# Performance work log

Measured on AMD Instinct MI355X. Metric: run time of the kernel, lower is better.

## Reference

```python
import jax, jax.numpy as jnp
import numpy as np

N_EMBD = 1024
N_HEAD = 16

def setup_inputs() -> dict:
    key = jax.random.key(0)
    k0, k1, k2, k3, k4 = jax.random.split(key, 5)
    scale = 1.0 / np.sqrt(N_EMBD)
    x = jax.random.normal(k0, (4, 2048, N_EMBD), dtype=jnp.float32)
    W_qkv = jax.random.normal(k1, (N_EMBD, 3 * N_EMBD), dtype=jnp.float32) * scale
    b_qkv = jax.random.normal(k2, (3 * N_EMBD,), dtype=jnp.float32) * 0.01
    W_proj = jax.random.normal(k3, (N_EMBD, N_EMBD), dtype=jnp.float32) * scale
    b_proj = jax.random.normal(k4, (N_EMBD,), dtype=jnp.float32) * 0.01
    return {"x": x, "W_qkv": W_qkv, "b_qkv": b_qkv, "W_proj": W_proj, "b_proj": b_proj}

def reference(x, W_qkv, b_qkv, W_proj, b_proj):
    B, S, E = x.shape
    H = N_HEAD
    D = E // H  # head dim
    kqv = x @ W_qkv + b_qkv  # [B,S,3E]
    k, q, v = jnp.split(kqv, 3, axis=-1)  # torch split order: k, q, v
    def to_heads(t):
        return t.reshape(B, S, H, D).transpose(0, 2, 1, 3)  # [B,H,S,D]
    k, q, v = to_heads(k), to_heads(q), to_heads(v)
    attn = jnp.einsum('bhqd,bhkd->bhqk', q, k) * (1.0 / np.sqrt(D))
    causal = jnp.tril(jnp.ones((S, S), dtype=bool))
    attn = jnp.where(causal, attn, -jnp.inf)
    attn = jax.nn.softmax(attn, axis=-1)
    # dropout is identity in eval mode (reference baseline)
    y = jnp.einsum('bhqk,bhkd->bhqd', attn, v)
    y = y.transpose(0, 2, 1, 3).reshape(B, S, E)
    return y @ W_proj + b_proj
```

## Files before the change

kernel.cpp:

```cpp
#include <hip/hip_runtime.h>
#include <hip/hip_bf16.h>

typedef __attribute__((ext_vector_type(8))) short  short8;
typedef __attribute__((ext_vector_type(4))) float  f32x4;
typedef __attribute__((ext_vector_type(4))) unsigned short u16x4;
typedef __attribute__((ext_vector_type(2))) unsigned int  uint32x2;

#define WAITVM(n) asm volatile("s_waitcnt vmcnt(" #n ")" ::: "memory")

__device__ __forceinline__ unsigned short f2bf(float f) {
    union { float f; unsigned int u; } c; c.f = f;
    unsigned int u = c.u + 0x7FFFu + ((c.u >> 16) & 1u);
    return (unsigned short)(u >> 16);
}

__device__ __forceinline__ unsigned int cvtpk_bf16(float lo, float hi) {
    unsigned int d;
    asm("v_cvt_pk_bf16_f32 %0, %1, %2" : "=v"(d) : "v"(lo), "v"(hi));
    return d;
}

__device__ __forceinline__ float exp2fast(float x) {
    float r;
    asm("v_exp_f32 %0, %1" : "=v"(r) : "v"(x));
    return r;
}

__device__ __forceinline__ void gll16(const void* g, void* lds) {
    __builtin_amdgcn_global_load_lds(
        (const __attribute__((address_space(1))) unsigned int*)g,
        (__attribute__((address_space(3))) unsigned int*)lds, 16, 0, 0);
}

__global__ void prep_kernel(const float* __restrict__ x, const float* __restrict__ Wq,
                            const float* __restrict__ Wp, unsigned short* __restrict__ xb,
                            unsigned short* __restrict__ WqT, unsigned short* __restrict__ WpT,
                            int nx) {
    const int blk = blockIdx.x;
    if (blk < 4096) {
        __shared__ float tile[32][33];
        const int cx = blk & 127;
        const int k0 = (blk >> 7) * 32;
        const float* W; unsigned short* Wt; int Nd, n0;
        if (cx < 96) { W = Wq; Wt = WqT; Nd = 3072; n0 = cx * 32; }
        else         { W = Wp; Wt = WpT; Nd = 1024; n0 = (cx - 96) * 32; }
        const int tx = threadIdx.x & 31, ty = threadIdx.x >> 5;
#pragma unroll
        for (int i = 0; i < 4; i++)
            tile[ty + i * 8][tx] = W[(size_t)(k0 + ty + i * 8) * Nd + n0 + tx];
        __syncthreads();
#pragma unroll
        for (int i = 0; i < 4; i++)
            Wt[(size_t)(n0 + ty + i * 8) * 1024 + k0 + tx] = f2bf(tile[tx][ty + i * 8]);
    } else {
        int i = ((blk - 4096) * 256 + threadIdx.x) * 4;
        if (i + 3 >= nx) return;
        float4 v = *(const float4*)(x + i);
        u16x4 o;
        o[0] = f2bf(v.x); o[1] = f2bf(v.y); o[2] = f2bf(v.z); o[3] = f2bf(v.w);
        *(u16x4*)(xb + i) = o;
    }
}

template <int BN, int MODE, int NT>
__global__ __launch_bounds__(512, 4) void gemmk64(
    const unsigned short* __restrict__ A,
    const unsigned short* __restrict__ Bt,
    const float* __restrict__ bias,
    float* __restrict__ Cf,
    unsigned short* __restrict__ kbuf,
    unsigned short* __restrict__ qbuf,
    unsigned short* __restrict__ vT,
    int M, int N, int K)
{
    constexpr int NF = BN / 64;
    constexpr int ABASE = 128 * 64;
    constexpr int SLOT = (128 + BN) * 64;
    __shared__ __align__(16) unsigned short lds[2][SLOT];

    const int tid = threadIdx.x;
    const int w = tid >> 6, lane = tid & 63;
    const int llo = lane & 15, lhi = lane >> 4;
    const int wm = w >> 2, wn = w & 3;

    const int nwg = gridDim.x * gridDim.y;
    const int bid = blockIdx.y * gridDim.x + blockIdx.x;
    const int wgid = (bid & 7) * (nwg >> 3) + (bid >> 3);
    const int mb = wgid / gridDim.x, nb = wgid - (wgid / gridDim.x) * gridDim.x;
    const int m0 = mb * 128, n0 = nb * BN;

    f32x4 acc[4][NF];
#pragma unroll
    for (int m = 0; m < 4; m++)
#pragma unroll
        for (int n = 0; n < NF; n++)
#pragma unroll
            for (int r = 0; r < 4; r++) acc[m][n][r] = 0.0f;

    const int gr8 = lane >> 3;
    const int swc = ((lane & 7) ^ gr8) * 8;
    const unsigned short* Asrc = A  + (size_t)(m0 + w * 16 + gr8) * K + swc;
    const unsigned short* Bsrc = Bt + (size_t)(n0 + w * 8 * NF + gr8) * K + swc;

    auto STAGE = [&](int sl_, int kt_) {
        unsigned short* sl = &lds[sl_][0];
        const size_t ko = (size_t)kt_ * 64;
        gll16(Asrc + ko,                 sl + (w * 16) * 64);
        gll16(Asrc + ko + 8 * (size_t)K, sl + (w * 16 + 8) * 64);
#pragma unroll
        for (int u = 0; u < NF; u++)
            gll16(Bsrc + ko + (size_t)(8 * u) * K, sl + ABASE + (w * 8 * NF + 8 * u) * 64);
    };

    STAGE(0, 0);

    const int sk = llo & 7;
    const int arow = (wm * 64 + llo) * 64;
    const int brow = ABASE + (wn * 16 * NF + llo) * 64;

    for (int kt = 0; kt < NT; ++kt) {
        WAITVM(0);
        __builtin_amdgcn_s_barrier();
        __builtin_amdgcn_sched_barrier(0);

        if (kt + 1 < NT) STAGE((kt + 1) & 1, kt + 1);

        const unsigned short* sa = &lds[kt & 1][0];

#pragma unroll
        for (int ks = 0; ks < 2; ks++) {
            const int pc = ((ks * 4 + lhi) ^ sk) * 8;
            short8 af[4], bv[NF];
#pragma unroll
            for (int m = 0; m < 4; m++) af[m] = *(const short8*)&sa[arow + m * 1024 + pc];
#pragma unroll
            for (int n = 0; n < NF; n++) bv[n] = *(const short8*)&sa[brow + n * 1024 + pc];

            __builtin_amdgcn_s_setprio(1);
#pragma unroll
            for (int m = 0; m < 4; m++)
#pragma unroll
                for (int n = 0; n < NF; n++)
                    acc[m][n] = __builtin_amdgcn_mfma_f32_16x16x32_bf16(af[m], bv[n], acc[m][n], 0, 0, 0);
            __builtin_amdgcn_s_setprio(0);
        }
    }

    if constexpr (MODE == 0) {
#pragma unroll
        for (int n = 0; n < NF; n++) {
            int col = n0 + wn * 16 * NF + n * 16 + llo;
            float bb = bias[col];
#pragma unroll
            for (int m = 0; m < 4; m++) {
                int row = m0 + wm * 64 + m * 16 + lhi * 4;
#pragma unroll
                for (int r = 0; r < 4; r++)
                    Cf[(size_t)(row + r) * N + col] = acc[m][n][r] + bb;
            }
        }
    } else {
#pragma unroll
        for (int n = 0; n < NF; n++) {
            int col = n0 + wn * 16 * NF + n * 16 + llo;
            int third = col >> 10;
            int cl  = col & 1023;
            float bb = bias[col];
            if (third == 2) {
#pragma unroll
                for (int m = 0; m < 4; m++) {
                    int row0 = m0 + wm * 64 + m * 16 + lhi * 4;
                    u16x4 pk;
#pragma unroll
                    for (int r = 0; r < 4; r++) pk[r] = f2bf(acc[m][n][r] + bb);
                    *(u16x4*)&vT[(size_t)cl * M + row0] = pk;
                }
            } else {
                unsigned short* dst = (third == 0) ? kbuf : qbuf;
                const float sc = (third == 1) ? 0.18033688f : 1.0f;
#pragma unroll
                for (int m = 0; m < 4; m++) {
                    int row0 = m0 + wm * 64 + m * 16 + lhi * 4;
#pragma unroll
                    for (int r = 0; r < 4; r++)
                        dst[(size_t)(row0 + r) * 1024 + cl] = f2bf((acc[m][n][r] + bb) * sc);
                }
            }
        }
    }
}

__global__ __launch_bounds__(256, 3) void attn_kernel(
    const unsigned short* __restrict__ K_,
    const unsigned short* __restrict__ Q_,
    const unsigned short* __restrict__ VT_,
    unsigned short* __restrict__ O,
    int S, int H, int M)
{
    const int E = 64 * H;
    const int tid = threadIdx.x;
    const int w = tid >> 6, lane = tid & 63;
    const int llo = lane & 15, lhi = lane >> 4;
    const int id = blockIdx.x;
    const int bh = id & 63;
    const int xi = id >> 6;
    const int b = bh >> 4, h = bh & 15;
    const int q0 = (15 - xi) * 128;

    __shared__ __align__(16) unsigned short kvlds[2][2][64 * 64];
    __shared__ __align__(16) unsigned short Ps[4][32 * 64];

    const int qw = q0 + w * 32;

    short8 qf[2][2];
#pragma unroll
    for (int m = 0; m < 2; m++)
#pragma unroll
        for (int kst = 0; kst < 2; kst++)
            qf[m][kst] = *(const short8*)(Q_ + (size_t)(b * S + qw + m * 16 + llo) * E
                                          + h * 64 + kst * 32 + lhi * 8);

    const short one_bf = (short)0x3F80;
    short8 ones = {one_bf, one_bf, one_bf, one_bf, one_bf, one_bf, one_bf, one_bf};

    f32x4 o[2][4];
    f32x4 lac[2];
#pragma unroll
    for (int m = 0; m < 2; m++) {
#pragma unroll
        for (int r = 0; r < 4; r++) lac[m][r] = 0.0f;
#pragma unroll
        for (int df = 0; df < 4; df++)
#pragma unroll
            for (int r = 0; r < 4; r++) o[m][df][r] = 0.0f;
    }

    const int gr = lane >> 3;
    const int gc = ((lane & 7) ^ gr) * 8;
    const unsigned short* ksp = K_  + (size_t)(b * S + w * 16 + gr) * E + h * 64 + gc;
    const unsigned short* vsp = VT_ + (size_t)(h * 64 + w * 16 + gr) * M + b * S + gc;
    unsigned short* kd = &kvlds[0][0][w * 16 * 64];
    unsigned short* vd = &kvlds[0][1][w * 16 * 64];

#define STAGE_KV(buf_, kv0_) {                                   \
        const size_t kro = (size_t)(kv0_) * E;                   \
        gll16(ksp + kro,           kd + (buf_) * 2 * 4096);      \
        gll16(ksp + kro + 8 * (size_t)E, kd + (buf_) * 2 * 4096 + 8 * 64); \
        gll16(vsp + (kv0_),        vd + (buf_) * 2 * 4096);      \
        gll16(vsp + (kv0_) + 8 * M, vd + (buf_) * 2 * 4096 + 8 * 64); \
    }

    STAGE_KV(0, 0);

    const int nt = q0 / 64 + 2;
    unsigned short* psw = &Ps[w][0];

    for (int t = 0; t < nt; ++t) {
        const int kv0 = t * 64;
        WAITVM(0);
        __builtin_amdgcn_s_barrier();
        __builtin_amdgcn_sched_barrier(0);

        if (t + 1 < nt) STAGE_KV((t + 1) & 1, kv0 + 64);

        const unsigned short* kb = &kvlds[t & 1][0][0];
        const unsigned short* vbuf = &kvlds[t & 1][1][0];

        if (kv0 <= qw + 31) {
            f32x4 st[2][4];
#pragma unroll
            for (int m = 0; m < 2; m++)
#pragma unroll
                for (int nf = 0; nf < 4; nf++)
#pragma unroll
                    for (int r = 0; r < 4; r++) st[m][nf][r] = 0.0f;

#pragma unroll
            for (int kst = 0; kst < 2; kst++) {
                const int pc = ((kst * 4 + lhi) ^ (llo & 7)) * 8;
                short8 kf[4];
#pragma unroll
                for (int nf = 0; nf < 4; nf++)
                    kf[nf] = *(const short8*)&kb[(nf * 16 + llo) * 64 + pc];
#pragma unroll
                for (int m = 0; m < 2; m++)
#pragma unroll
                    for (int nf = 0; nf < 4; nf++)
                        st[m][nf] = __builtin_amdgcn_mfma_f32_16x16x32_bf16(kf[nf], qf[m][kst], st[m][nf], 0, 0, 0);
            }

            const bool need_mask = (kv0 + 63 > qw);
#pragma unroll
            for (int m = 0; m < 2; m++) {
                const int qa = qw + m * 16 + llo;
                if (need_mask) {
#pragma unroll
                    for (int nf = 0; nf < 4; nf++)
#pragma unroll
                        for (int r = 0; r < 4; r++) {
                            int ka = kv0 + nf * 16 + lhi * 4 + r;
                            if (ka > qa) st[m][nf][r] = -1e30f;
                        }
                }
#pragma unroll
                for (int nf = 0; nf < 4; nf++) {
                    float p0 = exp2fast(st[m][nf][0]);
                    float p1 = exp2fast(st[m][nf][1]);
                    float p2 = exp2fast(st[m][nf][2]);
                    float p3 = exp2fast(st[m][nf][3]);
                    uint32x2 pk;
                    pk[0] = cvtpk_bf16(p0, p1);
                    pk[1] = cvtpk_bf16(p2, p3);
                    const int p16 = (nf * 2 + (lhi >> 1)) ^ (llo & 7);
                    *(uint32x2*)&psw[(m * 16 + llo) * 64 + p16 * 8 + (lhi & 1) * 4] = pk;
                }
            }

#pragma unroll
            for (int kst = 0; kst < 2; kst++) {
                const int pc = ((kst * 4 + lhi) ^ (llo & 7)) * 8;
                short8 pa[2], vb[4];
#pragma unroll
                for (int m = 0; m < 2; m++)
                    pa[m] = *(const short8*)&psw[(m * 16 + llo) * 64 + pc];
#pragma unroll
                for (int df = 0; df < 4; df++)
                    vb[df] = *(const short8*)&vbuf[(df * 16 + llo) * 64 + pc];
#pragma unroll
                for (int m = 0; m < 2; m++) {
#pragma unroll
                    for (int df = 0; df < 4; df++)
                        o[m][df] = __builtin_amdgcn_mfma_f32_16x16x32_bf16(pa[m], vb[df], o[m][df], 0, 0, 0);
                    lac[m] = __builtin_amdgcn_mfma_f32_16x16x32_bf16(pa[m], ones, lac[m], 0, 0, 0);
                }
            }
        }
    }
#undef STAGE_KV

#pragma unroll
    for (int m = 0; m < 2; m++)
#pragma unroll
        for (int r = 0; r < 4; r++) {
            float iv = 1.0f / lac[m][r];
            int q = qw + m * 16 + lhi * 4 + r;
#pragma unroll
            for (int df = 0; df < 4; df++)
                O[(size_t)(b * S + q) * E + h * 64 + df * 16 + llo] = f2bf(o[m][df][r] * iv);
        }
}

extern "C" void kernel_launch(void* const* d_in, const int* in_sizes, int n_in,
                              void* d_out, int out_size, void* d_ws, size_t ws_size,
                              hipStream_t stream) {
    const float* x      = (const float*)d_in[0];
    const float* W_qkv  = (const float*)d_in[1];
    const float* b_qkv  = (const float*)d_in[2];
    const float* W_proj = (const float*)d_in[3];
    const float* b_proj = (const float*)d_in[4];
    float* out = (float*)d_out;

    const int B = 4, S = 2048, E = 1024, H = 16;
    const int M = B * S;

    unsigned short* ws     = (unsigned short*)d_ws;
    unsigned short* xb     = ws;
    unsigned short* wqkvT  = xb + (size_t)M * E;
    unsigned short* wprojT = wqkvT + (size_t)3 * E * E;
    unsigned short* kbuf   = wprojT + (size_t)E * E;
    unsigned short* qbuf   = kbuf + (size_t)M * E;
    unsigned short* vTb    = qbuf + (size_t)M * E;
    unsigned short* obuf   = vTb + (size_t)M * E;

    const int nx = M * E;
    prep_kernel<<<dim3(4096 + nx / 1024), 256, 0, stream>>>(x, W_qkv, W_proj, xb, wqkvT, wprojT, nx);

    gemmk64<192, 1, 16><<<dim3(3 * E / 192, M / 128), 512, 0, stream>>>(
        xb, wqkvT, b_qkv, nullptr, kbuf, qbuf, vTb, M, 3 * E, E);
    attn_kernel<<<dim3(16 * B * H), 256, 0, stream>>>(kbuf, qbuf, vTb, obuf, S, H, M);
    gemmk64<128, 0, 16><<<dim3(E / 128, M / 128), 512, 0, stream>>>(
        obuf, wprojT, b_proj, out, nullptr, nullptr, nullptr, M, E, E);
}
```

Before: 138.7 us.

## Use 256x256-tile ping-pong GEMM kernel for QKV projection

Adds a new gemm256 kernel with 256x256 output tiles, double-buffered LDS and a fine-grained schedule that interleaves global-to-LDS loads with MFMA groups separated by barriers and raised wave priority. It also remaps workgroup IDs so that neighbouring blocks share operand tiles. It replaces the 128x192 tile kernel for the QKV GEMM to raise arithmetic intensity and overlap memory traffic with compute. The trade-off is more registers and LDS per block, so fewer blocks fit per CU, and a grid of only 384 blocks.

```diff
diff --git a/kernel.cpp b/kernel.cpp
--- a/kernel.cpp
+++ b/kernel.cpp
@@ -61,6 +61,173 @@
         *(u16x4*)(xb + i) = o;
     }
 }
+
+#define SA(b, ko, r) gll16(Asrc + (size_t)((r) * 64) * K + (ko), &lds[b][0][(r) * 4096 + w * 512])
+#define SB(b, ko, r) gll16(Bsrc + (size_t)((r) * 64) * K + (ko), &lds[b][1][(r) * 4096 + w * 512])
+#define BAR __builtin_amdgcn_s_barrier()
+#define LGKM0 { asm volatile("s_waitcnt lgkmcnt(0)" ::: "memory"); __builtin_amdgcn_sched_barrier(0); }
+#define LOADA(ab, MFG) { \
+    _Pragma("unroll") \
+    for (int m_ = 0; m_ < 4; m_++) { \
+        af[m_][0] = *(const short8*)&(ab)[(MFG) * 8192 + arow + m_ * 1024 + pc0]; \
+        af[m_][1] = *(const short8*)&(ab)[(MFG) * 8192 + arow + m_ * 1024 + pc1]; \
+    } }
+#define LOADB(dst, bb, NFG) { \
+    _Pragma("unroll") \
+    for (int n_ = 0; n_ < 2; n_++) { \
+        dst[n_][0] = *(const short8*)&(bb)[((NFG) * 2 + n_) * 4096 + brow + pc0]; \
+        dst[n_][1] = *(const short8*)&(bb)[((NFG) * 2 + n_) * 4096 + brow + pc1]; \
+    } }
+#define MMA(MFG, bv, NFG) { \
+    __builtin_amdgcn_s_setprio(1); \
+    _Pragma("unroll") \
+    for (int m_ = 0; m_ < 4; m_++) \
+        _Pragma("unroll") \
+        for (int n_ = 0; n_ < 2; n_++) { \
+            acc[(MFG) * 4 + m_][(NFG) * 2 + n_] = __builtin_amdgcn_mfma_f32_16x16x32_bf16( \
+                af[m_][0], bv[n_][0], acc[(MFG) * 4 + m_][(NFG) * 2 + n_], 0, 0, 0); \
+            acc[(MFG) * 4 + m_][(NFG) * 2 + n_] = __builtin_amdgcn_mfma_f32_16x16x32_bf16( \
+                af[m_][1], bv[n_][1], acc[(MFG) * 4 + m_][(NFG) * 2 + n_], 0, 0, 0); \
+        } \
+    __builtin_amdgcn_s_setprio(0); }
+
+template <int MODE>
+__global__ __launch_bounds__(512, 2) void gemm256(
+    const unsigned short* __restrict__ A,
+    const unsigned short* __restrict__ Bt,
+    const float* __restrict__ bias,
+    float* __restrict__ Cf,
+    unsigned short* __restrict__ kbuf,
+    unsigned short* __restrict__ qbuf,
+    unsigned short* __restrict__ vT,
+    int M, int N, int K)
+{
+    __shared__ __align__(16) unsigned short lds[2][2][16384];
+
+    const int tid = threadIdx.x;
+    const int w = tid >> 6, lane = tid & 63;
+    const int llo = lane & 15, lhi = lane >> 4;
+    const int wm = w >> 2, wn = w & 3;
+
+    const int nwg = gridDim.x * gridDim.y;
+    const int bid = blockIdx.y * gridDim.x + blockIdx.x;
+    const int wgid = (bid & 7) * (nwg >> 3) + (bid >> 3);
+    const int mb = wgid / gridDim.x, nb = wgid - (wgid / gridDim.x) * gridDim.x;
+    const int m0 = mb * 256, n0 = nb * 256;
+
+    f32x4 acc[8][4];
+#pragma unroll
+    for (int m = 0; m < 8; m++)
+#pragma unroll
+        for (int n = 0; n < 4; n++)
+#pragma unroll
+            for (int r = 0; r < 4; r++) acc[m][n][r] = 0.0f;
+
+    const int tr = tid >> 3, tc = tid & 7;
+    const int swz = (tc ^ (tr & 7)) * 8;
+    const unsigned short* Asrc = A + (size_t)(m0 + tr) * K + swz;
+    const unsigned short* Bsrc = Bt + (size_t)(n0 + tr) * K + swz;
+
+    SA(0, 0, 0); SA(0, 0, 1); SA(0, 0, 2); SA(0, 0, 3);
+    SB(0, 0, 0); SB(0, 0, 1); SB(0, 0, 2); SB(0, 0, 3);
+    SA(1, 64, 0); SA(1, 64, 1);
+    SB(1, 64, 0); SB(1, 64, 1);
+    WAITVM(4);
+    BAR;
+
+    const int kq = llo & 7;
+    const int pc0 = (lhi ^ kq) * 8;
+    const int pc1 = ((4 + lhi) ^ kq) * 8;
+    const int arow = (wm * 64 + llo) * 64;
+    const int brow = (wn * 16 + llo) * 64;
+
+    const unsigned short* A0 = &lds[0][0][0];
+    const unsigned short* B0 = &lds[0][1][0];
+    const unsigned short* A1 = &lds[1][0][0];
+    const unsigned short* B1 = &lds[1][1][0];
+
+    short8 af[4][2], bf0[2][2], bf1[2][2];
+
+    const int NIT = K >> 7;
+    for (int i = 0; i < NIT; ++i) {
+        const int k1 = (2 * i + 1) * 64, k2 = (2 * i + 2) * 64, k3 = (2 * i + 3) * 64;
+        const bool more = (i + 1 < NIT);
+
+        LOADA(A0, 0); LOADB(bf0, B0, 0);
+        SA(1, k1, 2); SA(1, k1, 3);
+        BAR; LGKM0; MMA(0, bf0, 0); BAR;
+        LOADB(bf1, B0, 1);
+        SB(1, k1, 2); SB(1, k1, 3);
+        BAR; LGKM0; MMA(0, bf1, 1); BAR;
+        LOADA(A0, 1);
+        if (more) { SA(0, k2, 0); SA(0, k2, 1); }
+        BAR; LGKM0; MMA(1, bf0, 0); BAR;
+        if (more) { SB(0, k2, 0); SB(0, k2, 1); WAITVM(4); } else { WAITVM(0); }
+        BAR; LGKM0; MMA(1, bf1, 1); BAR;
+        LOADA(A1, 0); LOADB(bf0, B1, 0);
+        if (more) { SA(0, k2, 2); SA(0, k2, 3); }
+        BAR; LGKM0; MMA(0, bf0, 0); BAR;
+        LOADB(bf1, B1, 1);
+        if (more) { SB(0, k2, 2); SB(0, k2, 3); }
+        BAR; LGKM0; MMA(0, bf1, 1); BAR;
+        LOADA(A1, 1);
+        if (more) { SA(1, k3, 0); SA(1, k3, 1); }
+        BAR; LGKM0; MMA(1, bf0, 0); BAR;
+        if (more) { SB(1, k3, 0); SB(1, k3, 1); WAITVM(4); }
+        BAR; LGKM0; MMA(1, bf1, 1); BAR;
+    }
+
+    if constexpr (MODE == 0) {
+#pragma unroll
+        for (int nf = 0; nf < 4; nf++) {
+            const int col = n0 + wn * 16 + nf * 64 + llo;
+            const float bb = bias[col];
+#pragma unroll
+            for (int mf = 0; mf < 8; mf++) {
+                const int row0 = m0 + wm * 64 + (mf & 3) * 16 + (mf >> 2) * 128 + lhi * 4;
+#pragma unroll
+                for (int r = 0; r < 4; r++)
+                    Cf[(size_t)(row0 + r) * N + col] = acc[mf][nf][r] + bb;
+            }
+        }
+    } else {
+#pragma unroll
+        for (int nf = 0; nf < 4; nf++) {
+            const int col = n0 + wn * 16 + nf * 64 + llo;
+            const int third = col >> 10;
+            const int cl = col & 1023;
+            const float bb = bias[col];
+            if (third == 2) {
+#pragma unroll
+                for (int mf = 0; mf < 8; mf++) {
+                    const int row0 = m0 + wm * 64 + (mf & 3) * 16 + (mf >> 2) * 128 + lhi * 4;
+                    u16x4 pk;
+#pragma unroll
+                    for (int r = 0; r < 4; r++) pk[r] = f2bf(acc[mf][nf][r] + bb);
+                    *(u16x4*)&vT[(size_t)cl * M + row0] = pk;
+                }
+            } else {
+                unsigned short* dst = (third == 0) ? kbuf : qbuf;
+                const float sc = (third == 1) ? 0.18033688f : 1.0f;
+#pragma unroll
+                for (int mf = 0; mf < 8; mf++) {
+                    const int row0 = m0 + wm * 64 + (mf & 3) * 16 + (mf >> 2) * 128 + lhi * 4;
+#pragma unroll
+                    for (int r = 0; r < 4; r++)
+                        dst[(size_t)(row0 + r) * 1024 + cl] = f2bf((acc[mf][nf][r] + bb) * sc);
+                }
+            }
+        }
+    }
+}
+
+#undef SA
+#undef SB
+#undef LOADA
+#undef LOADB
+#undef MMA
+#undef BAR
+#undef LGKM0
 
 template <int BN, int MODE, int NT>
 __global__ __launch_bounds__(512, 4) void gemmk64(
@@ -375,7 +542,7 @@
     const int nx = M * E;
     prep_kernel<<<dim3(4096 + nx / 1024), 256, 0, stream>>>(x, W_qkv, W_proj, xb, wqkvT, wprojT, nx);
 
-    gemmk64<192, 1, 16><<<dim3(3 * E / 192, M / 128), 512, 0, stream>>>(
+    gemm256<1><<<dim3(3 * E / 256, M / 256), 512, 0, stream>>>(
         xb, wqkvT, b_qkv, nullptr, kbuf, qbuf, vTb, M, 3 * E, E);
     attn_kernel<<<dim3(16 * B * H), 256, 0, stream>>>(kbuf, qbuf, vTb, obuf, S, H, M);
     gemmk64<128, 0, 16><<<dim3(E / 128, M / 128), 512, 0, stream>>>(
```

Measured after the change: 150.6 us. 1.09x slower.
